# Optimization experiments

Measured on AMD Instinct MI355X. Metric: run time of the kernel, lower is better.

Reference implementation:

```python
import jax, jax.numpy as jnp
import numpy as np

# (C,H,W) of x0..x11; flattened size +1 homogeneous coordinate per key
SHAPES = [(3,32,32),(96,32,32),(96,32,32),(96,16,16),(192,16,16),(192,16,16),(192,8,8),(192,8,8),(192,8,8),(640,1,1),(100,1,1),(10,1,1)]
# (Cin,Cout,k,stride,pad) for conv1..conv9
CONV = [(3,96,3,1,1),(96,96,3,1,1),(96,96,3,2,1),(96,192,3,1,1),(192,192,3,1,1),(192,192,3,2,1),(192,192,3,1,1),(192,192,1,1,0),(192,10,1,1,0)]
B = 128


def setup_inputs():
    key = jax.random.key(0)
    inp = {}
    k, key = jax.random.split(key)
    inp['x0'] = jax.random.normal(k, (int(np.prod(SHAPES[0])) + 1, B), jnp.float32)
    for i, s in enumerate(SHAPES):
        n = int(np.prod(s)) + 1
        k1, k2, key = jax.random.split(key, 3)
        inp['perm%d' % i] = jax.random.permutation(k1, n)
        inp['diag%d' % i] = jax.random.uniform(k2, (n,), jnp.float32, 0.5, 1.5)
    for j, (ci, co, ks, st, pd) in enumerate(CONV):
        k1, k2, key = jax.random.split(key, 3)
        inp['w%d' % (j + 1)] = jax.random.normal(k1, (co, ci, ks, ks), jnp.float32) / np.float32(np.sqrt(ci * ks * ks))
        inp['b%d' % (j + 1)] = jax.random.normal(k2, (co,), jnp.float32) * 0.01
    k1, k2, k3, k4 = jax.random.split(key, 4)
    inp['fw1'] = jax.random.normal(k1, (100, 640), jnp.float32) / np.float32(np.sqrt(640))
    inp['fb1'] = jax.random.normal(k2, (100,), jnp.float32) * 0.01
    inp['fw2'] = jax.random.normal(k3, (10, 100), jnp.float32) / np.float32(np.sqrt(100))
    inp['fb2'] = jax.random.normal(k4, (10,), jnp.float32) * 0.01
    return inp


def _decode(x, perm, diag):
    # A_inv @ x with A_inv = P^T D^{-1}; P^T gather index is argsort(perm)
    return (x / diag[:, None])[jnp.argsort(perm)]


def _encode(y, perm, diag):
    # A @ y with A = D P; (P y)[i] = y[perm[i]]
    return diag[:, None] * y[perm]


def _conv_aug(v, w, b, shape_in, stride, pad):
    # affine-augmented conv: [W b; 0 1] applied to [feat; t]
    C, H, Wd = shape_in
    feat, t = v[:-1], v[-1]                      # (C*H*W, B), (B,)
    x = feat.T.reshape(-1, C, H, Wd)
    y = jax.lax.conv_general_dilated(x, w, (stride, stride), [(pad, pad), (pad, pad)],
                                     dimension_numbers=('NCHW', 'OIHW', 'NCHW'))
    y = y + b[None, :, None, None] * t[:, None, None, None]
    yf = y.reshape(y.shape[0], -1).T             # (N_out, B)
    return jnp.concatenate([yf, t[None, :]], axis=0)


def _fc_aug(v, w, b):
    feat, t = v[:-1], v[-1]
    return jnp.concatenate([w @ feat + b[:, None] * t[None, :], t[None, :]], axis=0)


def _forward(x0, perms, diags, ws, bs, fw1, fb1, fw2, fb2):
    x = x0
    for i in range(9):
        v = _decode(x, perms[i], diags[i])
        y = _conv_aug(v, ws[i], bs[i], SHAPES[i], CONV[i][3], CONV[i][4])
        x = jax.nn.relu(_encode(y, perms[i + 1], diags[i + 1]))
    v = _decode(x, perms[9], diags[9])
    x = jax.nn.relu(_encode(_fc_aug(v, fw1, fb1), perms[10], diags[10]))
    v = _decode(x, perms[10], diags[10])
    return _encode(_fc_aug(v, fw2, fb2), perms[11], diags[11])


def reference(x0, perm0, perm1, perm2, perm3, perm4, perm5, perm6, perm7, perm8, perm9, perm10, perm11,
              diag0, diag1, diag2, diag3, diag4, diag5, diag6, diag7, diag8, diag9, diag10, diag11,
              w1, b1, w2, b2, w3, b3, w4, b4, w5, b5, w6, b6, w7, b7, w8, b8, w9, b9,
              fw1, fb1, fw2, fb2):
    perms = [perm0, perm1, perm2, perm3, perm4, perm5, perm6, perm7, perm8, perm9, perm10, perm11]
    diags = [diag0, diag1, diag2, diag3, diag4, diag5, diag6, diag7, diag8, diag9, diag10, diag11]
    ws = [w1, w2, w3, w4, w5, w6, w7, w8, w9]
    bs = [b1, b2, b3, b4, b5, b6, b7, b8, b9]
    return _forward(x0, perms, diags, ws, bs, fw1, fb1, fw2, fb2)
```

## Files before the change

### kernel.cpp

```cpp
#include <hip/hip_runtime.h>


#define B 128
#define ZPAD 2048

typedef _Float16 f16_t;
typedef __attribute__((ext_vector_type(8))) _Float16 f16x8;
typedef __attribute__((ext_vector_type(4))) _Float16 f16x4;
typedef __attribute__((ext_vector_type(4))) float f32x4;


__global__ void decode_kernel(const float* __restrict__ x, const int* __restrict__ perm,
                              const float* __restrict__ diag, float* __restrict__ v, int nrows) {
    int row = blockIdx.x * 8 + (threadIdx.x >> 5);
    if (row >= nrows) return;
    int lane = threadIdx.x & 31;
    int p = perm[row];
    float inv = 1.0f / diag[row];
    float4 val = ((const float4*)(x + (size_t)row * B))[lane];
    val.x *= inv; val.y *= inv; val.z *= inv; val.w *= inv;
    ((float4*)(v + (size_t)p * B))[lane] = val;
}

__global__ void encode_kernel(const float* __restrict__ y, const int* __restrict__ perm,
                              const float* __restrict__ diag, float* __restrict__ out, int nrows) {
    int row = blockIdx.x * 8 + (threadIdx.x >> 5);
    if (row >= nrows) return;
    int lane = threadIdx.x & 31;
    int p = perm[row];
    float d = diag[row];
    float4 val = ((const float4*)(y + (size_t)p * B))[lane];
    val.x *= d; val.y *= d; val.z *= d; val.w *= d;
    ((float4*)(out + (size_t)row * B))[lane] = val;
}

__global__ void fc_kernel(const float* __restrict__ v, const float* __restrict__ w,
                          const float* __restrict__ b, float* __restrict__ y,
                          int K, int R, int do_relu) {
    int r = blockIdx.x;
    int n = threadIdx.x;
    float t = v[(size_t)K * B + n];
    float val;
    if (r == R) {
        val = t;
    } else {
        float a0 = 0.f, a1 = 0.f, a2 = 0.f, a3 = 0.f;
        float a4 = 0.f, a5 = 0.f, a6 = 0.f, a7 = 0.f;
        const float* wr = w + (size_t)r * K;
        int k = 0;
        for (; k + 8 <= K; k += 8) {
            float4 w0 = *(const float4*)(wr + k);
            float4 w1 = *(const float4*)(wr + k + 4);
            float x0 = v[(size_t)(k + 0) * B + n];
            float x1 = v[(size_t)(k + 1) * B + n];
            float x2 = v[(size_t)(k + 2) * B + n];
            float x3 = v[(size_t)(k + 3) * B + n];
            float x4 = v[(size_t)(k + 4) * B + n];
            float x5 = v[(size_t)(k + 5) * B + n];
            float x6 = v[(size_t)(k + 6) * B + n];
            float x7 = v[(size_t)(k + 7) * B + n];
            a0 = fmaf(w0.x, x0, a0);
            a1 = fmaf(w0.y, x1, a1);
            a2 = fmaf(w0.z, x2, a2);
            a3 = fmaf(w0.w, x3, a3);
            a4 = fmaf(w1.x, x4, a4);
            a5 = fmaf(w1.y, x5, a5);
            a6 = fmaf(w1.z, x6, a6);
            a7 = fmaf(w1.w, x7, a7);
        }
        for (; k < K; ++k)
            a0 = fmaf(wr[k], v[(size_t)k * B + n], a0);
        val = b[r] * t + ((a0 + a1) + (a2 + a3)) + ((a4 + a5) + (a6 + a7));
    }
    if (do_relu) val = fmaxf(val, 0.f);
    y[(size_t)r * B + n] = val;
}


__global__ void pack_input_kernel(const float* __restrict__ v, f16_t* __restrict__ xout,
                                  float* __restrict__ tout) {
    int idx = blockIdx.x * 256 + threadIdx.x;
    int p = idx >> 7, n = idx & 127;
    f16x8 o = {};
    o[0] = (f16_t)v[(size_t)(0 * 1024 + p) * B + n];
    o[1] = (f16_t)v[(size_t)(1 * 1024 + p) * B + n];
    o[2] = (f16_t)v[(size_t)(2 * 1024 + p) * B + n];
    *(f16x8*)(xout + ZPAD + (size_t)p * 1024 + n * 8) = o;
    if (idx < B) tout[idx] = v[(size_t)3072 * B + idx];
}


struct WArgs {
    const float* w[9]; const float* b[9];
    int Ci[9], Co[9], KS[9], Cp[9], NCG[9];
    int woff[10]; int boff[10];
};

__global__ void pack_weights_kernel(WArgs A, f16_t* __restrict__ wp, float* __restrict__ bp,
                                    f16_t* __restrict__ x8a, f16_t* __restrict__ x8b) {
    int idx = blockIdx.x * 256 + threadIdx.x;
    if (idx < ZPAD) { x8a[idx] = (f16_t)0.f; x8b[idx] = (f16_t)0.f; }
    if (idx < A.boff[9]) {
        int l = 0;
        while (idx >= A.boff[l + 1]) ++l;
        int co = idx - A.boff[l];
        bp[idx] = (co < A.Co[l]) ? A.b[l][co] : 0.f;
    }
    if (idx >= A.woff[9]) return;
    int l = 0;
    while (idx >= A.woff[l + 1]) ++l;
    int e = idx - A.woff[l];
    int j = e & 7;
    int t1 = e >> 3;
    int Cp = A.Cp[l];
    int co = t1 % Cp;
    int gg = t1 / Cp;
    int ncg = A.NCG[l];
    int tap = gg / ncg, cg = gg - tap * ncg;
    int ks = A.KS[l];
    int kh = tap / ks, kw = tap - kh * ks;
    int ci = cg * 8 + j;
    float val = 0.f;
    if (co < A.Co[l] && tap < ks * ks && ci < A.Ci[l])
        val = A.w[l][(((size_t)co * A.Ci[l] + ci) * ks + kh) * ks + kw];
    wp[idx] = (f16_t)val;
}


template <int KS, int MS, bool F32OUT>
__global__ __launch_bounds__(256, (MS == 1) ? 3 : 2) void conv_mfma_kernel(
    const f16_t* __restrict__ xin, const float* __restrict__ t_in,
    const f16_t* __restrict__ wp, const float* __restrict__ bp,
    f16_t* __restrict__ xout, float* __restrict__ t_out, float* __restrict__ f32out,
    int Hi, int Wi, int Wo_log2, int HWo, int stride, int pad,
    int NCG, int nchunk, int KGr, int Co, int Co_pad, int PB8, int CB)
{
    const int wave = threadIdx.x >> 6;
    const int lane = threadIdx.x & 63;
    const int q = lane >> 4;
    const int r = lane & 15;

    const int gb  = blockIdx.x;
    const int xcd = gb & 7;
    const int j   = gb >> 3;
    const int cog = j % CB;
    const int pb  = xcd * PB8 + j / CB;

    const int p   = (MS == 4) ? (pb * 4 + wave) : pb;
    const int co0 = cog * 64 + ((MS == 1) ? wave * 16 : 0);

    const int ho = p >> Wo_log2;
    const int wo = p & ((1 << Wo_log2) - 1);
    const f16_t* xdata = xin + ZPAD;

    float tv[8];
#pragma unroll
    for (int ns = 0; ns < 8; ++ns) tv[ns] = t_in[ns * 16 + r];

    f32x4 acc[MS][8];
#pragma unroll
    for (int ms = 0; ms < MS; ++ms) {
        float4 b4 = *(const float4*)(bp + co0 + ms * 16 + q * 4);
#pragma unroll
        for (int ns = 0; ns < 8; ++ns) {
            acc[ms][ns][0] = b4.x * tv[ns];
            acc[ms][ns][1] = b4.y * tv[ns];
            acc[ms][ns][2] = b4.z * tv[ns];
            acc[ms][ns][3] = b4.w * tv[ns];
        }
    }

    const int hb = ho * stride - pad, wb = wo * stride - pad;

    int g = q, tap = 0, cg = q;
    while (cg >= NCG) { cg -= NCG; ++tap; }

    f16x8 bf0[8], bf1[8], af0[MS], af1[MS];

    auto loadB = [&](f16x8* bf) {
        int kh = 0, kw = 0;
        if (KS == 3) { kh = tap / 3; kw = tap - kh * 3; }
        int hi = hb + kh, wi = wb + kw;
        bool v = (g < KGr) & ((unsigned)hi < (unsigned)Hi) & ((unsigned)wi < (unsigned)Wi);
        int boff = ((cg * Hi + hi) * Wi + wi) << 10;
        const f16_t* bb = xdata + (v ? boff : -ZPAD) + r * 8;
#pragma unroll
        for (int ns = 0; ns < 8; ++ns) bf[ns] = *(const f16x8*)(bb + ns * 128);
    };
    auto loadA = [&](f16x8* af, int c) {
        int ac = c < nchunk ? c : nchunk - 1;
        const f16_t* ap = wp + (((ac * 4 + q) * Co_pad) + co0 + r) * 8;
#pragma unroll
        for (int ms = 0; ms < MS; ++ms) af[ms] = *(const f16x8*)(ap + ms * 128);
    };
    auto advance = [&]() {
        g += 4; cg += 4;
        while (cg >= NCG) { cg -= NCG; ++tap; }
    };
    auto domfma = [&](f16x8* af, f16x8* bf) {
#pragma unroll
        for (int ms = 0; ms < MS; ++ms)
#pragma unroll
            for (int ns = 0; ns < 8; ++ns)
                acc[ms][ns] = __builtin_amdgcn_mfma_f32_16x16x32_f16(af[ms], bf[ns], acc[ms][ns], 0, 0, 0);
    };

    loadB(bf0); loadA(af0, 0); advance();
    const int nck2 = (nchunk + 1) & ~1;
    for (int c = 0; c < nck2; c += 2) {
        loadB(bf1); loadA(af1, c + 1); advance();
        domfma(af0, bf0);
        loadB(bf0); loadA(af0, c + 2); advance();
        domfma(af1, bf1);
    }

    if (!F32OUT) {
#pragma unroll
        for (int ms = 0; ms < MS; ++ms) {
            int cob = co0 + ms * 16 + q * 4;
            if (cob < Co) {
                int off0 = ((cob >> 3) * HWo + p) * 1024 + (cob & 7) + r * 8;
#pragma unroll
                for (int ns = 0; ns < 8; ++ns) {
                    f16x4 h;
                    h[0] = (f16_t)fmaxf(acc[ms][ns][0], 0.f);
                    h[1] = (f16_t)fmaxf(acc[ms][ns][1], 0.f);
                    h[2] = (f16_t)fmaxf(acc[ms][ns][2], 0.f);
                    h[3] = (f16_t)fmaxf(acc[ms][ns][3], 0.f);
                    *(f16x4*)(xout + ZPAD + off0 + ns * 128) = h;
                }
            }
        }
        if (gb == 0 && threadIdx.x < B)
            t_out[threadIdx.x] = fmaxf(t_in[threadIdx.x], 0.f);
    } else {
#pragma unroll
        for (int ms = 0; ms < MS; ++ms)
#pragma unroll
            for (int ns = 0; ns < 8; ++ns)
#pragma unroll
                for (int e = 0; e < 4; ++e) {
                    int co = co0 + ms * 16 + q * 4 + e;
                    if (co < Co)
                        f32out[((size_t)co * HWo + p) * B + ns * 16 + r] =
                            fmaxf(acc[ms][ns][e], 0.f);
                }
        if (gb == 0 && threadIdx.x < B)
            f32out[(size_t)Co * HWo * B + threadIdx.x] = fmaxf(t_in[threadIdx.x], 0.f);
    }
}


extern "C" void kernel_launch(void* const* d_in, const int* in_sizes, int n_in,
                              void* d_out, int out_size, void* d_ws, size_t ws_size,
                              hipStream_t stream) {
    const float* x0 = (const float*)d_in[0];
    const int*   perm[12];
    const float* diag[12];
    for (int i = 0; i < 12; ++i) {
        perm[i] = (const int*)d_in[1 + 2 * i];
        diag[i] = (const float*)d_in[2 + 2 * i];
    }
    const float* wts[9];
    const float* bia[9];
    for (int j = 0; j < 9; ++j) {
        wts[j] = (const float*)d_in[25 + 2 * j];
        bia[j] = (const float*)d_in[26 + 2 * j];
    }
    const float* fw1 = (const float*)d_in[43];
    const float* fb1 = (const float*)d_in[44];
    const float* fw2 = (const float*)d_in[45];
    const float* fb2 = (const float*)d_in[46];
    float* out = (float*)d_out;

    static const int CiA[9]  = {3, 96, 96, 96, 192, 192, 192, 192, 192};
    static const int CoA[9]  = {96, 96, 96, 192, 192, 192, 192, 192, 10};
    static const int KSA[9]  = {3, 3, 3, 3, 3, 3, 3, 1, 1};
    static const int CpA[9]  = {128, 128, 128, 192, 192, 192, 192, 192, 64};
    static const int NCGA[9] = {1, 12, 12, 12, 24, 24, 24, 24, 24};
    static const int KGRA[9] = {9, 108, 108, 108, 216, 216, 216, 24, 24};
    static const int NCHK[9] = {3, 27, 27, 27, 54, 54, 54, 6, 6};
    static const int HiA[9]  = {32, 32, 32, 16, 16, 16, 8, 8, 8};
    static const int WoL[9]  = {5, 5, 4, 4, 4, 3, 3, 3, 3};
    static const int HWoA[9] = {1024, 1024, 256, 256, 256, 64, 64, 64, 64};
    static const int STA[9]  = {1, 1, 2, 1, 1, 2, 1, 1, 1};
    static const int PDA[9]  = {1, 1, 1, 1, 1, 1, 1, 0, 0};
    static const int MSA[9]  = {4, 4, 1, 1, 1, 1, 1, 1, 1};

    char* wsb = (char*)d_ws;
    const size_t BUF_F32  = 1574912;
    const size_t X8_BYTES = (size_t)(ZPAD + 12 * 1024 * 1024) * 2;
    float* bufA = (float*)wsb;
    float* bufB = (float*)(wsb + BUF_F32);
    f16_t* x8a  = (f16_t*)(wsb + 2 * BUF_F32);
    f16_t* x8b  = (f16_t*)(wsb + 2 * BUF_F32 + X8_BYTES);
    f16_t* wpb  = (f16_t*)(wsb + 2 * BUF_F32 + 2 * X8_BYTES);
    const size_t WP_BYTES = 2888704;
    float* bpb  = (float*)(wsb + 2 * BUF_F32 + 2 * X8_BYTES + WP_BYTES);
    float* t0   = (float*)((char*)bpb + 8192);
    float* t1   = t0 + 256;

    WArgs WA;
    int wo = 0, bo = 0;
    for (int l = 0; l < 9; ++l) {
        WA.w[l] = wts[l]; WA.b[l] = bia[l];
        WA.Ci[l] = CiA[l]; WA.Co[l] = CoA[l]; WA.KS[l] = KSA[l];
        WA.Cp[l] = CpA[l]; WA.NCG[l] = NCGA[l];
        WA.woff[l] = wo; wo += NCHK[l] * 4 * CpA[l] * 8;
        WA.boff[l] = bo; bo += CpA[l];
    }
    WA.woff[9] = wo; WA.boff[9] = bo;
    pack_weights_kernel<<<(wo + 255) / 256, 256, 0, stream>>>(WA, wpb, bpb, x8a, x8b);

    decode_kernel<<<(3073 + 7) / 8, 256, 0, stream>>>(x0, perm[0], diag[0], bufA, 3073);
    pack_input_kernel<<<131072 / 256, 256, 0, stream>>>(bufA, x8a, t0);

    f16_t* xin = x8a; f16_t* xout = x8b;
    float* tin = t0;  float* tout = t1;
    for (int l = 0; l < 9; ++l) {
        const int ms = MSA[l];
        const int PB = HWoA[l] / (ms == 4 ? 4 : 1);
        const int CB = CpA[l] / 64;
        dim3 grid(PB * CB);
        const int PB8 = PB / 8;
        const f16_t* wpl = wpb + WA.woff[l];
        const float* bpl = bpb + WA.boff[l];
        if (l <= 1) {
            conv_mfma_kernel<3, 4, false><<<grid, 256, 0, stream>>>(
                xin, tin, wpl, bpl, xout, tout, nullptr,
                HiA[l], HiA[l], WoL[l], HWoA[l], STA[l], PDA[l],
                NCGA[l], NCHK[l], KGRA[l], CoA[l], CpA[l], PB8, CB);
        } else if (l <= 6) {
            conv_mfma_kernel<3, 1, false><<<grid, 256, 0, stream>>>(
                xin, tin, wpl, bpl, xout, tout, nullptr,
                HiA[l], HiA[l], WoL[l], HWoA[l], STA[l], PDA[l],
                NCGA[l], NCHK[l], KGRA[l], CoA[l], CpA[l], PB8, CB);
        } else if (l == 7) {
            conv_mfma_kernel<1, 1, false><<<grid, 256, 0, stream>>>(
                xin, tin, wpl, bpl, xout, tout, nullptr,
                HiA[l], HiA[l], WoL[l], HWoA[l], STA[l], PDA[l],
                NCGA[l], NCHK[l], KGRA[l], CoA[l], CpA[l], PB8, CB);
        } else {
            conv_mfma_kernel<1, 1, true><<<grid, 256, 0, stream>>>(
                xin, tin, wpl, bpl, nullptr, nullptr, bufA,
                HiA[l], HiA[l], WoL[l], HWoA[l], STA[l], PDA[l],
                NCGA[l], NCHK[l], KGRA[l], CoA[l], CpA[l], PB8, CB);
        }
        f16_t* xt = xin; xin = xout; xout = xt;
        float* tt = tin; tin = tout; tout = tt;
    }

    fc_kernel<<<101, B, 0, stream>>>(bufA, fw1, fb1, bufB, 640, 100, 1);
    fc_kernel<<<11, B, 0, stream>>>(bufB, fw2, fb2, bufA, 100, 10, 0);
    encode_kernel<<<2, 256, 0, stream>>>(bufA, perm[11], diag[11], out, 11);
}
```

Before: 363.9 us.

## Split batch columns across blocks for small conv layers and deepen prefetch

Adds an NSPLIT template parameter so that layers 5-8, which have only 64 output positions, split the 128-column batch into two halves handled by separate blocks. This doubles the grid for those layers to fill more compute units. The software pipeline moves from a fixed two-stage double buffer to a PF-stage ring (three stages when MS=1). Tap and channel-group indexing becomes incremental with branchless wrap logic instead of division. The costs are more register pressure from the extra prefetch stage and weight loads repeated across the split blocks.

```diff
diff --git a/kernel.cpp b/kernel.cpp
--- a/kernel.cpp
+++ b/kernel.cpp
@@ -127,42 +127,48 @@
 }
 
 
-template <int KS, int MS, bool F32OUT>
+template <int KS, int MS, int NS, int NSPLIT, bool F32OUT>
 __global__ __launch_bounds__(256, (MS == 1) ? 3 : 2) void conv_mfma_kernel(
     const f16_t* __restrict__ xin, const float* __restrict__ t_in,
     const f16_t* __restrict__ wp, const float* __restrict__ bp,
     f16_t* __restrict__ xout, float* __restrict__ t_out, float* __restrict__ f32out,
-    int Hi, int Wi, int Wo_log2, int HWo, int stride, int pad,
-    int NCG, int nchunk, int KGr, int Co, int Co_pad, int PB8, int CB)
+    int Hi, int Wi, int Wo_log2, int HWo,
+    int stride, int pad, int NCG, int nchunk, int KGr, int Co, int Co_pad,
+    int PB8, int CB)
 {
+    constexpr int PF = (MS == 1) ? 3 : 2;
     const int wave = threadIdx.x >> 6;
     const int lane = threadIdx.x & 63;
     const int q = lane >> 4;
     const int r = lane & 15;
 
-    const int gb  = blockIdx.x;
+    const int gb = blockIdx.x;
     const int xcd = gb & 7;
-    const int j   = gb >> 3;
+    int j = gb >> 3;
+    int nh = 0;
+    if (NSPLIT == 2) { nh = j & 1; j >>= 1; }
     const int cog = j % CB;
     const int pb  = xcd * PB8 + j / CB;
 
     const int p   = (MS == 4) ? (pb * 4 + wave) : pb;
     const int co0 = cog * 64 + ((MS == 1) ? wave * 16 : 0);
+    const int ncol0 = nh * (NS * 16);
+    const int ncol8 = ncol0 * 8;
 
     const int ho = p >> Wo_log2;
     const int wo = p & ((1 << Wo_log2) - 1);
     const f16_t* xdata = xin + ZPAD;
 
-    float tv[8];
-#pragma unroll
-    for (int ns = 0; ns < 8; ++ns) tv[ns] = t_in[ns * 16 + r];
-
-    f32x4 acc[MS][8];
+    float tv[NS];
+#pragma unroll
+    for (int ns = 0; ns < NS; ++ns) tv[ns] = t_in[ncol0 + ns * 16 + r];
+
+    f32x4 acc[MS][NS];
 #pragma unroll
     for (int ms = 0; ms < MS; ++ms) {
         float4 b4 = *(const float4*)(bp + co0 + ms * 16 + q * 4);
 #pragma unroll
-        for (int ns = 0; ns < 8; ++ns) {
+        for (int ns = 0; ns < NS; ++ns) {
             acc[ms][ns][0] = b4.x * tv[ns];
             acc[ms][ns][1] = b4.y * tv[ns];
             acc[ms][ns][2] = b4.z * tv[ns];
@@ -171,47 +177,64 @@
     }
 
     const int hb = ho * stride - pad, wb = wo * stride - pad;
-
-    int g = q, tap = 0, cg = q;
-    while (cg >= NCG) { cg -= NCG; ++tap; }
-
-    f16x8 bf0[8], bf1[8], af0[MS], af1[MS];
-
-    auto loadB = [&](f16x8* bf) {
-        int kh = 0, kw = 0;
-        if (KS == 3) { kh = tap / 3; kw = tap - kh * 3; }
-        int hi = hb + kh, wi = wb + kw;
+    const int HiWi = Hi * Wi;
+    const int HiWi4 = 4 * HiWi;
+    const int NCGHW = NCG * HiWi;
+    const int wend = wb + KS;
+
+    int g = q, cg = q, hi = hb, wi = wb, cgHW;
+    {
+        while (cg >= NCG) { cg -= NCG; ++wi; if (wi == wend) { wi = wb; ++hi; } }
+        cgHW = cg * HiWi;
+    }
+
+    f16x8 bf[PF][NS], af[PF][MS];
+
+    auto advance = [&]() {
+        g += 4; cg += 4; cgHW += HiWi4;
+        if (NCG >= 4) {
+            int c2 = cg - NCG;
+            bool wrap = c2 >= 0;
+            int wn = wi + 1;
+            bool ww = wrap & (wn == wend);
+            cg   = wrap ? c2 : cg;
+            cgHW = wrap ? cgHW - NCGHW : cgHW;
+            wi   = wrap ? (ww ? wb : wn) : wi;
+            hi   = ww ? hi + 1 : hi;
+        } else {
+            while (cg >= NCG) { cg -= NCG; cgHW -= NCGHW; ++wi; if (wi == wend) { wi = wb; ++hi; } }
+        }
+    };
+    auto loadB = [&](f16x8* b) {
         bool v = (g < KGr) & ((unsigned)hi < (unsigned)Hi) & ((unsigned)wi < (unsigned)Wi);
-        int boff = ((cg * Hi + hi) * Wi + wi) << 10;
-        const f16_t* bb = xdata + (v ? boff : -ZPAD) + r * 8;
-#pragma unroll
-        for (int ns = 0; ns < 8; ++ns) bf[ns] = *(const f16x8*)(bb + ns * 128);
+        int boff = (cgHW + hi * Wi + wi) << 10;
+        const f16_t* bb = xdata + (v ? boff : -ZPAD) + ncol8 + r * 8;
+#pragma unroll
+        for (int ns = 0; ns < NS; ++ns) b[ns] = *(const f16x8*)(bb + ns * 128);
     };
-    auto loadA = [&](f16x8* af, int c) {
+    auto loadA = [&](f16x8* a, int c) {
         int ac = c < nchunk ? c : nchunk - 1;
         const f16_t* ap = wp + (((ac * 4 + q) * Co_pad) + co0 + r) * 8;
 #pragma unroll
-        for (int ms = 0; ms < MS; ++ms) af[ms] = *(const f16x8*)(ap + ms * 128);
+        for (int ms = 0; ms < MS; ++ms) a[ms] = *(const f16x8*)(ap + ms * 128);
     };
-    auto advance = [&]() {
-        g += 4; cg += 4;
-        while (cg >= NCG) { cg -= NCG; ++tap; }
+    auto domfma = [&](f16x8* a, f16x8* b) {
+#pragma unroll
+        for (int ms = 0; ms < MS; ++ms)
+#pragma unroll
+            for (int ns = 0; ns < NS; ++ns)
+                acc[ms][ns] = __builtin_amdgcn_mfma_f32_16x16x32_f16(a[ms], b[ns], acc[ms][ns], 0, 0, 0);
     };
-    auto domfma = [&](f16x8* af, f16x8* bf) {
-#pragma unroll
-        for (int ms = 0; ms < MS; ++ms)
-#pragma unroll
-            for (int ns = 0; ns < 8; ++ns)
-                acc[ms][ns] = __builtin_amdgcn_mfma_f32_16x16x32_f16(af[ms], bf[ns], acc[ms][ns], 0, 0, 0);
-    };
-
-    loadB(bf0); loadA(af0, 0); advance();
-    const int nck2 = (nchunk + 1) & ~1;
-    for (int c = 0; c < nck2; c += 2) {
-        loadB(bf1); loadA(af1, c + 1); advance();
-        domfma(af0, bf0);
-        loadB(bf0); loadA(af0, c + 2); advance();
-        domfma(af1, bf1);
+
+#pragma unroll
+    for (int pf = 0; pf < PF; ++pf) { loadB(bf[pf]); loadA(af[pf], pf); advance(); }
+    const int nck = ((nchunk + PF - 1) / PF) * PF;
+    for (int c = 0; c < nck; c += PF) {
+#pragma unroll
+        for (int pf = 0; pf < PF; ++pf) {
+            domfma(af[pf], bf[pf]);
+            loadB(bf[pf]); loadA(af[pf], c + PF + pf); advance();
+        }
     }
 
     if (!F32OUT) {
@@ -219,9 +242,9 @@
         for (int ms = 0; ms < MS; ++ms) {
             int cob = co0 + ms * 16 + q * 4;
             if (cob < Co) {
-                int off0 = ((cob >> 3) * HWo + p) * 1024 + (cob & 7) + r * 8;
-#pragma unroll
-                for (int ns = 0; ns < 8; ++ns) {
+                int off0 = ((cob >> 3) * HWo + p) * 1024 + (cob & 7) + ncol8 + r * 8;
+#pragma unroll
+                for (int ns = 0; ns < NS; ++ns) {
                     f16x4 h;
                     h[0] = (f16_t)fmaxf(acc[ms][ns][0], 0.f);
                     h[1] = (f16_t)fmaxf(acc[ms][ns][1], 0.f);
@@ -237,12 +260,12 @@
 #pragma unroll
         for (int ms = 0; ms < MS; ++ms)
 #pragma unroll
-            for (int ns = 0; ns < 8; ++ns)
+            for (int ns = 0; ns < NS; ++ns)
 #pragma unroll
                 for (int e = 0; e < 4; ++e) {
                     int co = co0 + ms * 16 + q * 4 + e;
                     if (co < Co)
-                        f32out[((size_t)co * HWo + p) * B + ns * 16 + r] =
+                        f32out[((size_t)co * HWo + p) * B + ncol0 + ns * 16 + r] =
                             fmaxf(acc[ms][ns][e], 0.f);
                 }
         if (gb == 0 && threadIdx.x < B)
@@ -286,6 +309,7 @@
     static const int STA[9]  = {1, 1, 2, 1, 1, 2, 1, 1, 1};
     static const int PDA[9]  = {1, 1, 1, 1, 1, 1, 1, 0, 0};
     static const int MSA[9]  = {4, 4, 1, 1, 1, 1, 1, 1, 1};
+    static const int NSPL[9] = {1, 1, 1, 1, 1, 2, 2, 2, 2};
 
     char* wsb = (char*)d_ws;
     const size_t BUF_F32  = 1574912;
@@ -320,28 +344,33 @@
     for (int l = 0; l < 9; ++l) {
         const int ms = MSA[l];
         const int PB = HWoA[l] / (ms == 4 ? 4 : 1);
+        const int PB8 = PB / 8;
         const int CB = CpA[l] / 64;
-        dim3 grid(PB * CB);
-        const int PB8 = PB / 8;
+        dim3 grid(8 * PB8 * CB * NSPL[l]);
         const f16_t* wpl = wpb + WA.woff[l];
         const float* bpl = bpb + WA.boff[l];
         if (l <= 1) {
-            conv_mfma_kernel<3, 4, false><<<grid, 256, 0, stream>>>(
+            conv_mfma_kernel<3, 4, 8, 1, false><<<grid, 256, 0, stream>>>(
                 xin, tin, wpl, bpl, xout, tout, nullptr,
                 HiA[l], HiA[l], WoL[l], HWoA[l], STA[l], PDA[l],
                 NCGA[l], NCHK[l], KGRA[l], CoA[l], CpA[l], PB8, CB);
+        } else if (l <= 4) {
+            conv_mfma_kernel<3, 1, 8, 1, false><<<grid, 256, 0, stream>>>(
+                xin, tin, wpl, bpl, xout, tout, nullptr,
+                HiA[l], HiA[l], WoL[l], HWoA[l], STA[l], PDA[l],
+                NCGA[l], NCHK[l], KGRA[l], CoA[l], CpA[l], PB8, CB);
         } else if (l <= 6) {
-            conv_mfma_kernel<3, 1, false><<<grid, 256, 0, stream>>>(
+            conv_mfma_kernel<3, 1, 4, 2, false><<<grid, 256, 0, stream>>>(
                 xin, tin, wpl, bpl, xout, tout, nullptr,
                 HiA[l], HiA[l], WoL[l], HWoA[l], STA[l], PDA[l],
                 NCGA[l], NCHK[l], KGRA[l], CoA[l], CpA[l], PB8, CB);
         } else if (l == 7) {
-            conv_mfma_kernel<1, 1, false><<<grid, 256, 0, stream>>>(
+            conv_mfma_kernel<1, 1, 4, 2, false><<<grid, 256, 0, stream>>>(
                 xin, tin, wpl, bpl, xout, tout, nullptr,
                 HiA[l], HiA[l], WoL[l], HWoA[l], STA[l], PDA[l],
                 NCGA[l], NCHK[l], KGRA[l], CoA[l], CpA[l], PB8, CB);
         } else {
-            conv_mfma_kernel<1, 1, true><<<grid, 256, 0, stream>>>(
+            conv_mfma_kernel<1, 1, 4, 2, true><<<grid, 256, 0, stream>>>(
                 xin, tin, wpl, bpl, nullptr, nullptr, bufA,
                 HiA[l], HiA[l], WoL[l], HWoA[l], STA[l], PDA[l],
                 NCGA[l], NCHK[l], KGRA[l], CoA[l], CpA[l], PB8, CB);
```

Measured after the change: 374.3 us. +2.9%, slower.
